# Optimization experiments

Measured on AMD Instinct MI355X. Metric: run time of the kernel, lower is better.

## Reference

```python
import jax, jax.numpy as jnp
import numpy as np

INPUT_SIZE = 1024
HIDDEN = [2048, 2048]
OUTPUT_SIZE = 10
N = 16384
PRIOR_VAR = 100.0


def setup_inputs() -> dict:
    key = jax.random.key(0)
    ks = jax.random.split(key, 8)
    X = jax.random.normal(ks[0], (N, INPUT_SIZE), dtype=jnp.float32)
    Y = jax.random.randint(ks[1], (N,), 0, OUTPUT_SIZE, dtype=jnp.int32)
    # Kaiming-ish init like nn.Linear defaults (scale irrelevant to correctness)
    def lin(k, fan_in, fan_out):
        bound = 1.0 / np.sqrt(fan_in)
        kw, kb = jax.random.split(k)
        W = jax.random.uniform(kw, (fan_out, fan_in), jnp.float32, -bound, bound)
        b = jax.random.uniform(kb, (fan_out,), jnp.float32, -bound, bound)
        return W, b
    W1, b1 = lin(ks[2], INPUT_SIZE, HIDDEN[0])
    W2, b2 = lin(ks[3], HIDDEN[0], HIDDEN[1])
    W3, b3 = lin(ks[4], HIDDEN[1], OUTPUT_SIZE)
    return {"X": X, "Y": Y, "W1": W1, "b1": b1, "W2": W2, "b2": b2, "W3": W3, "b3": b3}


def reference(X, Y, W1, b1, W2, b2, W3, b3):
    # Batched version of the per-sample Linear+ReLU+...+Linear+Softmax(dim=0) loop.
    h = jax.nn.relu(X @ W1.T + b1)            # [N, H0]
    h = jax.nn.relu(h @ W2.T + b2)            # [N, H1]
    logits = h @ W3.T + b3                    # [N, C]
    # Categorical(probs=softmax(logits)).log_prob(Y[i]) == log_softmax(logits)[i, Y[i]]
    logp = jax.nn.log_softmax(logits, axis=-1)
    log_likelihood = jnp.sum(jnp.take_along_axis(logp, Y[:, None].astype(jnp.int32), axis=-1))
    # MVN(0, 100*I) log-prob over flattened params: closed-form diagonal Gaussian.
    params = (W1, b1, W2, b2, W3, b3)
    d = sum(p.size for p in params)
    sq = sum(jnp.sum(p * p) for p in params)
    log_prior = -0.5 * (sq / PRIOR_VAR + d * jnp.log(2.0 * jnp.pi * PRIOR_VAR))
    return log_likelihood + log_prior
```

## Files before the change

kernel.cpp:

```cpp
#include <hip/hip_runtime.h>
#include <math.h>

typedef __bf16 bf16;
typedef bf16 bf16x8 __attribute__((ext_vector_type(8)));
typedef bf16 bf16x4 __attribute__((ext_vector_type(4)));
typedef float f32x4 __attribute__((ext_vector_type(4)));

#define NROWS 16384
#define HID 2048

__device__ __forceinline__ void gload_lds16(const bf16* g, bf16* l) {
  __builtin_amdgcn_global_load_lds((const __attribute__((address_space(1))) void*)g,
                                   (__attribute__((address_space(3))) void*)l,
                                   16, 0, 0);
}

#define MF(a, b, c) __builtin_amdgcn_mfma_f32_16x16x32_bf16((a), (b), (c), 0, 0, 0)

#define BAR()                                  \
  asm volatile("" ::: "memory");               \
  __builtin_amdgcn_s_barrier();                \
  asm volatile("" ::: "memory");

#define LGKM0()                                           \
  asm volatile("s_waitcnt lgkmcnt(0)" ::: "memory");      \
  __builtin_amdgcn_sched_barrier(0);

template <int K, bool RELU>
__global__ __launch_bounds__(512, 2) void gemm256(const bf16* __restrict__ A,
                                                  const bf16* __restrict__ B,
                                                  const float* __restrict__ bias,
                                                  bf16* __restrict__ C, int N) {
  extern __shared__ bf16 smem[];
  constexpr int NT = K / 32;
  const int tid = threadIdx.x;
  const int lane = tid & 63;
  const int w = tid >> 6;
  const int wr = w >> 2, wc = w & 3;

  const int xc = blockIdx.x & 7, xl = blockIdx.x >> 3;
  const int bm = xc * 8 + (xl >> 3);
  const int bn = xl & 7;

  const bf16* Abase = A + (size_t)bm * 256 * K;
  const bf16* Bbase = B + (size_t)bn * 256 * K;

  const int r0 = tid >> 2;
  const int r1 = r0 + 128;
  const int kp = tid & 3;
  const size_t offS0 = (size_t)r0 * K + ((kp ^ ((r0 >> 1) & 3)) * 8);
  const size_t offS1 = (size_t)r1 * K + ((kp ^ ((r1 >> 1) & 3)) * 8);

  int offRA[8], offRB[4];
  const int kk = lane >> 4;
#pragma unroll
  for (int mi = 0; mi < 8; ++mi) {
    const int r = wr * 128 + mi * 16 + (lane & 15);
    offRA[mi] = (r * 4 + (kk ^ ((r >> 1) & 3))) * 8;
  }
#pragma unroll
  for (int ni = 0; ni < 4; ++ni) {
    const int r = wc * 64 + ni * 16 + (lane & 15);
    offRB[ni] = (r * 4 + (kk ^ ((r >> 1) & 3))) * 8 + 8192;
  }

  f32x4 acc[8][4] = {};
  bf16x8 a0[4], a1[4], b0[4], b1[4];

#define LD8(off) (*(const bf16x8*)(smem + (off)))

#define STAGE(t, b)                                                   \
  {                                                                   \
    const bf16* As = Abase + (size_t)(t) * 32;                        \
    const bf16* Bs = Bbase + (size_t)(t) * 32;                        \
    bf16* d = smem + (b) * 16384 + w * 512;    \
    gload_lds16(As + offS0, d);                                       \
    gload_lds16(As + offS1, d + 4096);                                \
    gload_lds16(Bs + offS0, d + 8192);                                \
    gload_lds16(Bs + offS1, d + 12288);                               \
  }

#define MFMA16(AV, BV, mh)                                           \
  __builtin_amdgcn_s_setprio(1);                                     \
  acc[(mh)*4+0][0] = MF(AV[0], BV[0], acc[(mh)*4+0][0]);             \
  acc[(mh)*4+0][1] = MF(AV[0], BV[1], acc[(mh)*4+0][1]);             \
  acc[(mh)*4+0][2] = MF(AV[0], BV[2], acc[(mh)*4+0][2]);             \
  acc[(mh)*4+0][3] = MF(AV[0], BV[3], acc[(mh)*4+0][3]);             \
  acc[(mh)*4+1][0] = MF(AV[1], BV[0], acc[(mh)*4+1][0]);             \
  acc[(mh)*4+1][1] = MF(AV[1], BV[1], acc[(mh)*4+1][1]);             \
  acc[(mh)*4+1][2] = MF(AV[1], BV[2], acc[(mh)*4+1][2]);             \
  acc[(mh)*4+1][3] = MF(AV[1], BV[3], acc[(mh)*4+1][3]);             \
  acc[(mh)*4+2][0] = MF(AV[2], BV[0], acc[(mh)*4+2][0]);             \
  acc[(mh)*4+2][1] = MF(AV[2], BV[1], acc[(mh)*4+2][1]);             \
  acc[(mh)*4+2][2] = MF(AV[2], BV[2], acc[(mh)*4+2][2]);             \
  acc[(mh)*4+2][3] = MF(AV[2], BV[3], acc[(mh)*4+2][3]);             \
  acc[(mh)*4+3][0] = MF(AV[3], BV[0], acc[(mh)*4+3][0]);             \
  acc[(mh)*4+3][1] = MF(AV[3], BV[1], acc[(mh)*4+3][1]);             \
  acc[(mh)*4+3][2] = MF(AV[3], BV[2], acc[(mh)*4+3][2]);             \
  acc[(mh)*4+3][3] = MF(AV[3], BV[3], acc[(mh)*4+3][3]);             \
  __builtin_amdgcn_s_setprio(0);

  STAGE(0, 0); STAGE(1, 1); STAGE(2, 2);
  asm volatile("s_waitcnt vmcnt(8)" ::: "memory");
  BAR();
  {
#pragma unroll
    for (int i = 0; i < 4; ++i) b0[i] = LD8(offRB[i]);
#pragma unroll
    for (int i = 0; i < 4; ++i) a0[i] = LD8(offRA[i]);
  }

  for (int t = 0; t < NT; t += 2) {
    if (t + 3 < NT) STAGE(t + 3, (t + 3) & 3);
    {
      const int bb = (t & 3) * 16384;
#pragma unroll
      for (int i = 0; i < 4; ++i) a1[i] = LD8(bb + offRA[4 + i]);
    }
    MFMA16(a0, b0, 0);
    LGKM0();
    if (t + 3 < NT)      asm volatile("s_waitcnt vmcnt(8)" ::: "memory");
    else if (t + 2 < NT) asm volatile("s_waitcnt vmcnt(4)" ::: "memory");
    else                 asm volatile("s_waitcnt vmcnt(0)" ::: "memory");
    BAR();
    {
      const int nb = ((t + 1) & 3) * 16384;
#pragma unroll
      for (int i = 0; i < 4; ++i) b1[i] = LD8(nb + offRB[i]);
#pragma unroll
      for (int i = 0; i < 4; ++i) a0[i] = LD8(nb + offRA[i]);
    }
    MFMA16(a1, b0, 1);

    if (t + 4 < NT) STAGE(t + 4, (t + 4) & 3);
    {
      const int bb = ((t + 1) & 3) * 16384;
#pragma unroll
      for (int i = 0; i < 4; ++i) a1[i] = LD8(bb + offRA[4 + i]);
    }
    MFMA16(a0, b1, 0);
    LGKM0();
    if (t + 4 < NT)      asm volatile("s_waitcnt vmcnt(8)" ::: "memory");
    else if (t + 3 < NT) asm volatile("s_waitcnt vmcnt(4)" ::: "memory");
    else                 asm volatile("s_waitcnt vmcnt(0)" ::: "memory");
    if (t + 2 < NT) {
      BAR();
      const int nb = ((t + 2) & 3) * 16384;
#pragma unroll
      for (int i = 0; i < 4; ++i) b0[i] = LD8(nb + offRB[i]);
#pragma unroll
      for (int i = 0; i < 4; ++i) a0[i] = LD8(nb + offRA[i]);
    }
    MFMA16(a1, b1, 1);
  }

  const int crow0 = bm * 256 + wr * 128 + (lane >> 4) * 4;
  const int ccol0 = bn * 256 + wc * 64 + (lane & 15);
#pragma unroll
  for (int mi = 0; mi < 8; ++mi) {
#pragma unroll
    for (int ni = 0; ni < 4; ++ni) {
      const int col = ccol0 + ni * 16;
      const float bvv = bias[col];
#pragma unroll
      for (int j = 0; j < 4; ++j) {
        const int row = crow0 + mi * 16 + j;
        float v = acc[mi][ni][j] + bvv;
        if (RELU) v = fmaxf(v, 0.f);
        C[(size_t)row * N + col] = (bf16)v;
      }
    }
  }
}

struct CvtSqArgs {
  const float* src[6];
  bf16* dst[6];
  int n4[6];
  int dosq[6];
};

__global__ __launch_bounds__(256) void cvtsq_kernel(CvtSqArgs a, float* __restrict__ acc) {
  float s = 0.f;
  const int S = gridDim.x * blockDim.x;
  const int gid = blockIdx.x * blockDim.x + threadIdx.x;
#pragma unroll 1
  for (int seg = 0; seg < 6; ++seg) {
    const float4* __restrict__ src = (const float4*)a.src[seg];
    bf16x4* __restrict__ dst = (bf16x4*)a.dst[seg];
    const int n4 = a.n4[seg];
    const bool dq = a.dosq[seg] != 0;
    const int nb = n4 & ~(4 * S - 1);
    for (int i = gid; i < nb; i += 4 * S) {
      float4 v0 = src[i];
      float4 v1 = src[i + S];
      float4 v2 = src[i + 2 * S];
      float4 v3 = src[i + 3 * S];
      if (dst) {
        bf16x4 o0, o1, o2, o3;
        o0[0]=(bf16)v0.x; o0[1]=(bf16)v0.y; o0[2]=(bf16)v0.z; o0[3]=(bf16)v0.w;
        o1[0]=(bf16)v1.x; o1[1]=(bf16)v1.y; o1[2]=(bf16)v1.z; o1[3]=(bf16)v1.w;
        o2[0]=(bf16)v2.x; o2[1]=(bf16)v2.y; o2[2]=(bf16)v2.z; o2[3]=(bf16)v2.w;
        o3[0]=(bf16)v3.x; o3[1]=(bf16)v3.y; o3[2]=(bf16)v3.z; o3[3]=(bf16)v3.w;
        dst[i] = o0; dst[i + S] = o1; dst[i + 2 * S] = o2; dst[i + 3 * S] = o3;
      }
      if (dq) {
        s += v0.x*v0.x + v0.y*v0.y + v0.z*v0.z + v0.w*v0.w;
        s += v1.x*v1.x + v1.y*v1.y + v1.z*v1.z + v1.w*v1.w;
        s += v2.x*v2.x + v2.y*v2.y + v2.z*v2.z + v2.w*v2.w;
        s += v3.x*v3.x + v3.y*v3.y + v3.z*v3.z + v3.w*v3.w;
      }
    }
    for (int i = nb + gid; i < n4; i += S) {
      float4 v = src[i];
      if (dst) {
        bf16x4 o;
        o[0]=(bf16)v.x; o[1]=(bf16)v.y; o[2]=(bf16)v.z; o[3]=(bf16)v.w;
        dst[i] = o;
      }
      if (dq) s += v.x*v.x + v.y*v.y + v.z*v.z + v.w*v.w;
    }
  }
#pragma unroll
  for (int off = 32; off; off >>= 1) s += __shfl_xor(s, off, 64);
  if ((threadIdx.x & 63) == 0) atomicAdd(&acc[1], s);
}

__global__ __launch_bounds__(256) void loss_kernel(const bf16* __restrict__ h2,
                                                   const bf16* __restrict__ W3b,
                                                   const float* __restrict__ b3,
                                                   const int* __restrict__ Y,
                                                   float* __restrict__ acc) {
  __shared__ bf16 w3s[10 * HID];
  for (int i = threadIdx.x; i < 10 * HID / 8; i += 256)
    ((bf16x8*)w3s)[i] = ((const bf16x8*)W3b)[i];
  __syncthreads();

  const int lane = threadIdx.x & 63;
  const int w = threadIdx.x >> 6;
  const int nwave = gridDim.x * 4;
  float lsum = 0.f;

  for (int row = blockIdx.x * 4 + w; row < NROWS; row += nwave) {
    float p[10];
#pragma unroll
    for (int c = 0; c < 10; ++c) p[c] = 0.f;
    const bf16* hrow = h2 + (size_t)row * HID;
#pragma unroll
    for (int it = 0; it < 4; ++it) {
      const int k = it * 512 + lane * 8;
      bf16x8 hv = *(const bf16x8*)&hrow[k];
      float hf[8];
#pragma unroll
      for (int j = 0; j < 8; ++j) hf[j] = (float)hv[j];
#pragma unroll
      for (int c = 0; c < 10; ++c) {
        bf16x8 wv = *(const bf16x8*)&w3s[c * HID + k];
        float dp = 0.f;
#pragma unroll
        for (int j = 0; j < 8; ++j) dp += hf[j] * (float)wv[j];
        p[c] += dp;
      }
    }
#pragma unroll
    for (int off = 32; off; off >>= 1)
#pragma unroll
      for (int c = 0; c < 10; ++c) p[c] += __shfl_xor(p[c], off, 64);

    float lg[10], m = -1e30f;
#pragma unroll
    for (int c = 0; c < 10; ++c) { lg[c] = p[c] + b3[c]; m = fmaxf(m, lg[c]); }
    float s = 0.f;
#pragma unroll
    for (int c = 0; c < 10; ++c) s += expf(lg[c] - m);
    const float lse = m + logf(s);
    const int y = Y[row];
    float ly = 0.f;
#pragma unroll
    for (int c = 0; c < 10; ++c) ly += (c == y) ? lg[c] : 0.f;
    lsum += ly - lse;
  }
  if (lane == 0) atomicAdd(&acc[0], lsum);
}

__global__ void finalize_kernel(float* __restrict__ out, const float* __restrict__ acc,
                                const float* __restrict__ b3, double dterm) {
  double sq = (double)acc[1];
  for (int i = 0; i < 10; ++i) sq += (double)b3[i] * (double)b3[i];
  out[0] = (float)((double)acc[0] - 0.5 * (sq / 100.0 + dterm));
}

extern "C" void kernel_launch(void* const* d_in, const int* in_sizes, int n_in,
                              void* d_out, int out_size, void* d_ws, size_t ws_size,
                              hipStream_t stream) {
  const float* X  = (const float*)d_in[0];
  const int*   Y  = (const int*)d_in[1];
  const float* W1 = (const float*)d_in[2];
  const float* b1 = (const float*)d_in[3];
  const float* W2 = (const float*)d_in[4];
  const float* b2 = (const float*)d_in[5];
  const float* W3 = (const float*)d_in[6];
  const float* b3 = (const float*)d_in[7];
  float* out = (float*)d_out;

  char* ws = (char*)d_ws;
  size_t off = 0;
  auto alloc = [&](size_t bytes) -> void* {
    void* p = ws + off;
    off += (bytes + 255) & ~(size_t)255;
    return p;
  };
  bf16* Xb  = (bf16*)alloc((size_t)NROWS * 1024 * 2);
  bf16* W1b = (bf16*)alloc((size_t)HID * 1024 * 2);
  bf16* W2b = (bf16*)alloc((size_t)HID * HID * 2);
  bf16* W3b = (bf16*)alloc((size_t)10 * HID * 2);
  bf16* h1  = (bf16*)alloc((size_t)NROWS * HID * 2);
  bf16* h2  = (bf16*)alloc((size_t)NROWS * HID * 2);
  float* acc = (float*)alloc(256);

  hipMemsetAsync(acc, 0, 16, stream);

  CvtSqArgs ca;
  ca.src[0] = X;  ca.dst[0] = Xb;  ca.n4[0] = NROWS * 1024 / 4; ca.dosq[0] = 0;
  ca.src[1] = W1; ca.dst[1] = W1b; ca.n4[1] = HID * 1024 / 4;   ca.dosq[1] = 1;
  ca.src[2] = W2; ca.dst[2] = W2b; ca.n4[2] = HID * HID / 4;    ca.dosq[2] = 1;
  ca.src[3] = W3; ca.dst[3] = W3b; ca.n4[3] = 10 * HID / 4;     ca.dosq[3] = 1;
  ca.src[4] = b1; ca.dst[4] = nullptr; ca.n4[4] = HID / 4;      ca.dosq[4] = 1;
  ca.src[5] = b2; ca.dst[5] = nullptr; ca.n4[5] = HID / 4;      ca.dosq[5] = 1;
  cvtsq_kernel<<<512, 256, 0, stream>>>(ca, acc);

  hipFuncSetAttribute((const void*)gemm256<1024, true>,
                      hipFuncAttributeMaxDynamicSharedMemorySize, 131072);
  hipFuncSetAttribute((const void*)gemm256<2048, true>,
                      hipFuncAttributeMaxDynamicSharedMemorySize, 131072);

  gemm256<1024, true><<<512, 512, 131072, stream>>>(Xb, W1b, b1, h1, HID);
  gemm256<2048, true><<<512, 512, 131072, stream>>>(h1, W2b, b2, h2, HID);

  loss_kernel<<<1024, 256, 0, stream>>>(h2, W3b, b3, Y, acc);

  long long d = 0;
  for (int i = 2; i < 8; ++i) d += in_sizes[i];
  double dterm = (double)d * log(2.0 * M_PI * 100.0);
  finalize_kernel<<<1, 1, 0, stream>>>(out, acc, b3, dterm);
}
```

Before: 416.5 us.

## Restructure GEMM main loop into four-phase interleaved load/MFMA schedule

Replaces the two-tile unrolled ping-pong loop with a one-tile-per-iteration loop split into four phases. Each phase issues one global-to-LDS stage op, loads a quarter of the A/B fragments from LDS, and runs 8 MFMAs, with barriers between phases. The aim is to interleave global loads, LDS reads and matrix ops more finely, in the style of 8-wave ping-pong schedules. It adds many more barriers per K step, which may serialize waves and lower MFMA throughput.

```diff
diff --git a/kernel.cpp b/kernel.cpp
--- a/kernel.cpp
+++ b/kernel.cpp
@@ -65,93 +65,77 @@
   }
 
   f32x4 acc[8][4] = {};
-  bf16x8 a0[4], a1[4], b0[4], b1[4];
+  bf16x8 aU[4], aL[4], bL[2], bR[2];
 
 #define LD8(off) (*(const bf16x8*)(smem + (off)))
 
-#define STAGE(t, b)                                                   \
-  {                                                                   \
-    const bf16* As = Abase + (size_t)(t) * 32;                        \
-    const bf16* Bs = Bbase + (size_t)(t) * 32;                        \
-    bf16* d = smem + (b) * 16384 + w * 512;    \
-    gload_lds16(As + offS0, d);                                       \
-    gload_lds16(As + offS1, d + 4096);                                \
-    gload_lds16(Bs + offS0, d + 8192);                                \
-    gload_lds16(Bs + offS1, d + 12288);                               \
-  }
-
-#define MFMA16(AV, BV, mh)                                           \
-  __builtin_amdgcn_s_setprio(1);                                     \
-  acc[(mh)*4+0][0] = MF(AV[0], BV[0], acc[(mh)*4+0][0]);             \
-  acc[(mh)*4+0][1] = MF(AV[0], BV[1], acc[(mh)*4+0][1]);             \
-  acc[(mh)*4+0][2] = MF(AV[0], BV[2], acc[(mh)*4+0][2]);             \
-  acc[(mh)*4+0][3] = MF(AV[0], BV[3], acc[(mh)*4+0][3]);             \
-  acc[(mh)*4+1][0] = MF(AV[1], BV[0], acc[(mh)*4+1][0]);             \
-  acc[(mh)*4+1][1] = MF(AV[1], BV[1], acc[(mh)*4+1][1]);             \
-  acc[(mh)*4+1][2] = MF(AV[1], BV[2], acc[(mh)*4+1][2]);             \
-  acc[(mh)*4+1][3] = MF(AV[1], BV[3], acc[(mh)*4+1][3]);             \
-  acc[(mh)*4+2][0] = MF(AV[2], BV[0], acc[(mh)*4+2][0]);             \
-  acc[(mh)*4+2][1] = MF(AV[2], BV[1], acc[(mh)*4+2][1]);             \
-  acc[(mh)*4+2][2] = MF(AV[2], BV[2], acc[(mh)*4+2][2]);             \
-  acc[(mh)*4+2][3] = MF(AV[2], BV[3], acc[(mh)*4+2][3]);             \
-  acc[(mh)*4+3][0] = MF(AV[3], BV[0], acc[(mh)*4+3][0]);             \
-  acc[(mh)*4+3][1] = MF(AV[3], BV[1], acc[(mh)*4+3][1]);             \
-  acc[(mh)*4+3][2] = MF(AV[3], BV[2], acc[(mh)*4+3][2]);             \
-  acc[(mh)*4+3][3] = MF(AV[3], BV[3], acc[(mh)*4+3][3]);             \
+#define STAGE1(t, b, op)                                                     \
+  {                                                                          \
+    bf16* d = smem + (b) * 16384 + (op) * 4096 + w * 512;                    \
+    const bf16* g = ((op) < 2 ? Abase : Bbase) + (size_t)(t) * 32 +          \
+                    (((op) & 1) ? offS1 : offS0);                            \
+    gload_lds16(g, d);                                                       \
+  }
+
+#define STAGE(t, b)                                                          \
+  STAGE1(t, b, 0) STAGE1(t, b, 1) STAGE1(t, b, 2) STAGE1(t, b, 3)
+
+#define MF8(AV, BV, mh, nh)                                                  \
+  __builtin_amdgcn_s_setprio(1);                                             \
+  acc[(mh)*4+0][(nh)*2+0] = MF(AV[0], BV[0], acc[(mh)*4+0][(nh)*2+0]);       \
+  acc[(mh)*4+0][(nh)*2+1] = MF(AV[0], BV[1], acc[(mh)*4+0][(nh)*2+1]);       \
+  acc[(mh)*4+1][(nh)*2+0] = MF(AV[1], BV[0], acc[(mh)*4+1][(nh)*2+0]);       \
+  acc[(mh)*4+1][(nh)*2+1] = MF(AV[1], BV[1], acc[(mh)*4+1][(nh)*2+1]);       \
+  acc[(mh)*4+2][(nh)*2+0] = MF(AV[2], BV[0], acc[(mh)*4+2][(nh)*2+0]);       \
+  acc[(mh)*4+2][(nh)*2+1] = MF(AV[2], BV[1], acc[(mh)*4+2][(nh)*2+1]);       \
+  acc[(mh)*4+3][(nh)*2+0] = MF(AV[3], BV[0], acc[(mh)*4+3][(nh)*2+0]);       \
+  acc[(mh)*4+3][(nh)*2+1] = MF(AV[3], BV[1], acc[(mh)*4+3][(nh)*2+1]);       \
   __builtin_amdgcn_s_setprio(0);
 
   STAGE(0, 0); STAGE(1, 1); STAGE(2, 2);
   asm volatile("s_waitcnt vmcnt(8)" ::: "memory");
   BAR();
-  {
-#pragma unroll
-    for (int i = 0; i < 4; ++i) b0[i] = LD8(offRB[i]);
-#pragma unroll
-    for (int i = 0; i < 4; ++i) a0[i] = LD8(offRA[i]);
-  }
-
-  for (int t = 0; t < NT; t += 2) {
-    if (t + 3 < NT) STAGE(t + 3, (t + 3) & 3);
-    {
-      const int bb = (t & 3) * 16384;
-#pragma unroll
-      for (int i = 0; i < 4; ++i) a1[i] = LD8(bb + offRA[4 + i]);
-    }
-    MFMA16(a0, b0, 0);
+
+  for (int t = 0; t < NT; ++t) {
+    const int bb = (t & 3) * 16384;
+    const int sb = (t + 3) & 3;
+    const bool st = (t + 3) < NT;
+
+    if (st) STAGE1(t + 3, sb, 0);
+#pragma unroll
+    for (int i = 0; i < 4; ++i) aU[i] = LD8(bb + offRA[i]);
+#pragma unroll
+    for (int i = 0; i < 2; ++i) bL[i] = LD8(bb + offRB[i]);
+    BAR();
     LGKM0();
-    if (t + 3 < NT)      asm volatile("s_waitcnt vmcnt(8)" ::: "memory");
-    else if (t + 2 < NT) asm volatile("s_waitcnt vmcnt(4)" ::: "memory");
-    else                 asm volatile("s_waitcnt vmcnt(0)" ::: "memory");
-    BAR();
-    {
-      const int nb = ((t + 1) & 3) * 16384;
-#pragma unroll
-      for (int i = 0; i < 4; ++i) b1[i] = LD8(nb + offRB[i]);
-#pragma unroll
-      for (int i = 0; i < 4; ++i) a0[i] = LD8(nb + offRA[i]);
-    }
-    MFMA16(a1, b0, 1);
-
-    if (t + 4 < NT) STAGE(t + 4, (t + 4) & 3);
-    {
-      const int bb = ((t + 1) & 3) * 16384;
-#pragma unroll
-      for (int i = 0; i < 4; ++i) a1[i] = LD8(bb + offRA[4 + i]);
-    }
-    MFMA16(a0, b1, 0);
+    MF8(aU, bL, 0, 0);
+    BAR();
+
+    if (st) STAGE1(t + 3, sb, 1);
+#pragma unroll
+    for (int i = 0; i < 4; ++i) aL[i] = LD8(bb + offRA[4 + i]);
+    BAR();
     LGKM0();
-    if (t + 4 < NT)      asm volatile("s_waitcnt vmcnt(8)" ::: "memory");
-    else if (t + 3 < NT) asm volatile("s_waitcnt vmcnt(4)" ::: "memory");
-    else                 asm volatile("s_waitcnt vmcnt(0)" ::: "memory");
-    if (t + 2 < NT) {
-      BAR();
-      const int nb = ((t + 2) & 3) * 16384;
-#pragma unroll
-      for (int i = 0; i < 4; ++i) b0[i] = LD8(nb + offRB[i]);
-#pragma unroll
-      for (int i = 0; i < 4; ++i) a0[i] = LD8(nb + offRA[i]);
-    }
-    MFMA16(a1, b1, 1);
+    MF8(aL, bL, 1, 0);
+    BAR();
+
+    if (st) STAGE1(t + 3, sb, 2);
+#pragma unroll
+    for (int i = 0; i < 2; ++i) bR[i] = LD8(bb + offRB[2 + i]);
+    BAR();
+    LGKM0();
+    MF8(aU, bR, 0, 1);
+    BAR();
+
+    if (st) STAGE1(t + 3, sb, 3);
+    BAR();
+    MF8(aL, bR, 1, 1);
+    if (t + 1 < NT) {
+      if (t + 3 < NT)      asm volatile("s_waitcnt vmcnt(8)" ::: "memory");
+      else if (t + 2 < NT) asm volatile("s_waitcnt vmcnt(4)" ::: "memory");
+      else                 asm volatile("s_waitcnt vmcnt(0)" ::: "memory");
+    }
+    BAR();
   }
 
   const int crow0 = bm * 256 + wr * 128 + (lane >> 4) * 4;
```

Result: slower. 437.5 us (+5.0%).
